# Kernel tuning notes

Measured on AMD Instinct MI355X. Metric: run time of the kernel, lower is better.

Reference implementation:

```python
import jax, jax.numpy as jnp
import numpy as np

SCALE = 2  # init_kwargs scale


def _splits(a, s):
    # (..., W, H) -> (..., W//s, H//s, s*s), matching torch view/permute order
    *lead, W, H = a.shape
    Ws, Hs = W // s, H // s
    n = len(lead)
    b = a.reshape(*lead, s, Ws, s, Hs)
    b = jnp.transpose(b, tuple(range(n)) + (n + 1, n + 3, n, n + 2))
    return b.reshape(*lead, Ws, Hs, s * s)


def _p2o(psf, shape):
    # point-spread-function -> optical transfer function (zero-pad, center-roll, fft2)
    k1, k2 = psf.shape[-2], psf.shape[-1]
    otf = jnp.zeros(psf.shape[:-2] + shape, psf.dtype).at[..., :k1, :k2].set(psf)
    otf = jnp.roll(otf, (-(k1 // 2), -(k2 // 2)), axis=(-2, -1))
    return jnp.fft.fft2(otf, axes=(-2, -1))


def _upsample_zeros(x, s):
    if s == 1:
        return x
    B, C, H, W = x.shape
    return jnp.zeros((B, C, H * s, W * s), x.dtype).at[..., ::s, ::s].set(x)


def setup_inputs() -> dict:
    key = jax.random.key(0)
    k1, k2 = jax.random.split(key)
    B, C, H, W, K = 4, 64, 128, 128, 5
    x = jax.random.normal(k1, (B, C, H, W), jnp.float32)
    w = jax.random.normal(k2, (1, C, K, K), jnp.float32)
    # module init applies softmax over flattened kernel
    weight = jax.nn.softmax(w.reshape(1, C, -1), axis=-1).reshape(1, C, K, K)
    bias = jnp.zeros((1, C, 1, 1), jnp.float32)
    lambda_reg = jnp.full((1, 1, 1, 1), 0.1, jnp.float32)
    return {"x": x, "weight": weight, "bias": bias, "lambda_reg": lambda_reg}


def reference(x, weight, bias, lambda_reg):
    s = SCALE
    _, _, h, w = x.shape
    STy = _upsample_zeros(x, s)                      # [B,C,h*s,w*s] zero-interleaved
    if s != 1:
        x0 = jnp.repeat(jnp.repeat(x, s, axis=-2), s, axis=-1)  # nearest interp
    else:
        x0 = x
    FB = _p2o(weight, (h * s, w * s))                # [1,C,hs,ws] complex
    FBC = jnp.conj(FB)
    F2B = jnp.abs(FB) ** 2
    FBFy = FBC * jnp.fft.fft2(STy, axes=(-2, -1))
    FR = FBFy + jnp.fft.fft2(lambda_reg * x0, axes=(-2, -1))
    FBR = jnp.mean(_splits(FB * FR, s), axis=-1)     # [B,C,h,w] complex
    invW = jnp.mean(_splits(F2B, s), axis=-1)        # [1,C,h,w] real
    lambda_small = lambda_reg                        # scalar lambda: no split needed
    invWBR = FBR / (invW + lambda_small)
    FCBinvWBR = FBC * jnp.tile(invWBR, (1, 1, s, s))
    FX = (FR - FCBinvWBR) / lambda_reg
    out = jnp.real(jnp.fft.ifft2(FX, axes=(-2, -1)))
    return out + bias
```

## Files before the change

kernel.cpp:

```cpp
#include <hip/hip_runtime.h>
#include <math.h>


struct cx { float x, y; };
__device__ __forceinline__ cx cmul(cx a, cx b){ return cx{a.x*b.x - a.y*b.y, a.x*b.y + a.y*b.x}; }
__device__ __forceinline__ cx cadd(cx a, cx b){ return cx{a.x+b.x, a.y+b.y}; }
__device__ __forceinline__ cx csub(cx a, cx b){ return cx{a.x-b.x, a.y-b.y}; }
__device__ __forceinline__ cx cconj(cx a){ return cx{a.x, -a.y}; }
__device__ __forceinline__ cx cscale(cx a, float s){ return cx{a.x*s, a.y*s}; }

__device__ __forceinline__ float2 cmulf(float2 a, float2 b){
    return make_float2(a.x*b.x - a.y*b.y, a.x*b.y + a.y*b.x);
}
__device__ __forceinline__ float2 cmulcf(float2 a, float2 b){
    return make_float2(a.x*b.x + a.y*b.y, a.y*b.x - a.x*b.y);
}
__device__ __forceinline__ float2 caddf(float2 a, float2 b){ return make_float2(a.x+b.x, a.y+b.y); }
__device__ __forceinline__ float2 csubf(float2 a, float2 b){ return make_float2(a.x-b.x, a.y-b.y); }

__device__ __forceinline__ cx conjpair(cx w, float2 A, float2 B){
    return cx{ w.x*(A.x+B.x) + w.y*(A.y-B.y),
               w.x*(A.y+B.y) - w.y*(A.x-B.x) };
}

__device__ __forceinline__ void barrier_lds(){
    __builtin_amdgcn_sched_barrier(0);
    asm volatile("s_waitcnt lgkmcnt(0)" ::: "memory");
    __builtin_amdgcn_s_barrier();
    __builtin_amdgcn_sched_barrier(0);
}

__global__ __launch_bounds__(256)
void precompute_K(const float* __restrict__ weight, const float* __restrict__ lam_ptr,
                  float2* __restrict__ KA, float2* __restrict__ KB)
{
    __shared__ float2 P[5 * 256];

    const int tid  = threadIdx.x;
    const int c    = blockIdx.x >> 5;
    const int slab = blockIdx.x & 31;

    const float* wc = weight + c*25;
    const float lam = lam_ptr[0];
    const float inv_lam = 1.0f / lam;
    const float th  = -6.28318530717958647692f * (1.0f/256.0f);

    {
        float s1,c1, s2,c2;
        __sincosf(th * (float)tid,     &s1, &c1);
        __sincosf(th * (float)(2*tid), &s2, &c2);
        cx er[5] = { cx{c2,-s2}, cx{c1,-s1}, cx{1.f,0.f}, cx{c1,s1}, cx{c2,s2} };
        const int rs = (tid >> 1) | ((tid & 1) << 7);
        #pragma unroll
        for (int a = 0; a < 5; ++a) {
            float px = 0.f, py = 0.f;
            #pragma unroll
            for (int b = 0; b < 5; ++b) {
                float w = wc[a*5 + b];
                px += w * er[b].x;
                py += w * er[b].y;
            }
            P[a*256 + rs] = make_float2(px, py);
        }
    }
    __syncthreads();

    const float scale = 1.0f / 65536.0f;

    #pragma unroll 1
    for (int it = 0; it < 2; ++it) {
        const int p  = slab*512 + it*256 + tid;
        const int qb = p >> 7, rb = p & 127;
        const int q = (int)(__brev((unsigned)qb) >> 25);
        const int r = (int)(__brev((unsigned)rb) >> 25);
        const int rr = (r >> 1) | ((r & 1) << 7);

        float sq1,cq1, sq2,cq2, sr1,cr1;
        __sincosf(th * (float)q,     &sq1, &cq1);
        __sincosf(th * (float)(2*q), &sq2, &cq2);
        __sincosf(th * (float)r,     &sr1, &cr1);
        const cx w1{cq1, sq1};
        const cx w2{cq2, sq2};
        const cx wr{cr1, sr1};

        float2 p0_0 = P[0*256+rr], p1_0 = P[0*256+rr+64];
        float2 p0_1 = P[1*256+rr], p1_1 = P[1*256+rr+64];
        float2 p0_2 = P[2*256+rr], p1_2 = P[2*256+rr+64];
        float2 p0_3 = P[3*256+rr], p1_3 = P[3*256+rr+64];
        float2 p0_4 = P[4*256+rr], p1_4 = P[4*256+rr+64];
        cx B1 = conjpair(w1, p0_1, p0_3);
        cx B2 = conjpair(w2, p0_0, p0_4);
        cx m0 = cx{p0_2.x, p0_2.y};
        cx F00 = cadd(cadd(m0, B1), B2);
        cx F10 = cadd(csub(m0, B1), B2);
        cx D1 = conjpair(w1, p1_1, p1_3);
        cx D2 = conjpair(w2, p1_0, p1_4);
        cx m1 = cx{p1_2.x, p1_2.y};
        cx F01 = cadd(cadd(m1, D1), D2);
        cx F11 = cadd(csub(m1, D1), D2);

        float SF2 = F00.x*F00.x + F00.y*F00.y + F01.x*F01.x + F01.y*F01.y
                  + F10.x*F10.x + F10.y*F10.y + F11.x*F11.x + F11.y*F11.y;
        cx Du0{1.f+cq1,  sq1}, Du1{1.f-cq1, -sq1};
        cx Dv0{1.f+cr1,  sr1}, Dv1{1.f-cr1, -sr1};
        cx T = cadd(cmul(Du0, cadd(cmul(F00,Dv0), cmul(F01,Dv1))),
                    cmul(Du1, cadd(cmul(F10,Dv0), cmul(F11,Dv1))));
        float invW = 0.25f * SF2;
        cx M{invW + 0.25f*lam*T.x, 0.25f*lam*T.y};
        float idn = 1.0f / (invW + lam);
        cx V{M.x*idn, M.y*idn};
        cx W{(1.f - V.x)*inv_lam, -V.y*inv_lam};

        cx Sa = cadd(F00,F01), Sb = cadd(F10,F11);
        cx Da = csub(F00,F01), Db = csub(F10,F11);
        cx C00 = cadd(Sa,Sb), C10 = csub(Sa,Sb);
        cx C01 = cadd(Da,Db), C11 = csub(Da,Db);

        cx WR  = cmul(W,  cconj(wr));
        cx WQ  = cmul(W,  cconj(w1));
        cx WQR = cmul(WQ, cconj(wr));
        cx H0 = cadd(cmul(cconj(C00), W  ), cx{4.f,0.f});
        cx H1 = cadd(cmul(cconj(C01), WR ), cx{4.f,0.f});
        cx H2 = cadd(cmul(cconj(C10), WQ ), cx{4.f,0.f});
        cx H3 = cadd(cmul(cconj(C11), WQR), cx{4.f,0.f});

        float2 kAv = make_float2((H0.x - H1.y)*scale, (H0.y + H1.x)*scale);
        float2 kBv = make_float2((H2.x - H3.y)*scale, (H2.y + H3.x)*scale);
        const int o = (c << 14) + p;
        KA[o] = kAv;
        KB[o] = kBv;
    }
}

#define ST2 129

template<int AXIS> __device__ __forceinline__ int laddr(int line, int i){
    return AXIS ? (i*ST2 + line) : (line*ST2 + i);
}

template<int AXIS, int S>
__device__ __forceinline__ void fwd_pair(float2* Sm, const float2* TW, int tid)
{
    const int h  = 64 >> S;
    const int hh = 32 >> S;
    #pragma unroll
    for (int it = 0; it < 4; ++it) {
        int qid  = it*1024 + tid;
        int line = qid & 127;
        int t    = qid >> 7;
        int blk  = t >> (5 - S);
        int j    = t & (hh - 1);
        int i0   = (blk << (7 - S)) + j;
        int a0 = laddr<AXIS>(line, i0);
        int a1 = laddr<AXIS>(line, i0 + hh);
        int a2 = laddr<AXIS>(line, i0 + h);
        int a3 = laddr<AXIS>(line, i0 + h + hh);
        float2 e0 = Sm[a0], e1 = Sm[a1], e2 = Sm[a2], e3 = Sm[a3];
        float2 w0 = TW[j << S], w1 = TW[(j << S) + 32], w2 = TW[j << (S + 1)];
        float2 u0 = caddf(e0, e2), d0 = cmulf(csubf(e0, e2), w0);
        float2 u1 = caddf(e1, e3), d1 = cmulf(csubf(e1, e3), w1);
        Sm[a0] = caddf(u0, u1);
        Sm[a1] = cmulf(csubf(u0, u1), w2);
        Sm[a2] = caddf(d0, d1);
        Sm[a3] = cmulf(csubf(d0, d1), w2);
    }
}

template<int AXIS, int S>
__device__ __forceinline__ void inv_pair(float2* Sm, const float2* TW, int tid)
{
    const int h = 1 << S;
    #pragma unroll
    for (int it = 0; it < 4; ++it) {
        int qid  = it*1024 + tid;
        int line = qid & 127;
        int t    = qid >> 7;
        int blk  = t >> S;
        int j    = t & (h - 1);
        int base = (blk << (S + 2)) + j;
        int a0 = laddr<AXIS>(line, base);
        int a1 = laddr<AXIS>(line, base + h);
        int a2 = laddr<AXIS>(line, base + 2*h);
        int a3 = laddr<AXIS>(line, base + 3*h);
        float2 e0 = Sm[a0], e1 = Sm[a1], e2 = Sm[a2], e3 = Sm[a3];
        float2 cw0 = TW[j << (6 - S)];
        float2 cw1 = TW[j << (5 - S)];
        float2 cw2 = TW[(j << (5 - S)) + 32];
        float2 t1 = cmulcf(e1, cw0);
        float2 A0 = caddf(e0, t1), A1 = csubf(e0, t1);
        float2 t2 = cmulcf(e3, cw0);
        float2 A2 = caddf(e2, t2), A3 = csubf(e2, t2);
        float2 u = cmulcf(A2, cw1);
        Sm[a0] = caddf(A0, u);
        Sm[a2] = csubf(A0, u);
        float2 v = cmulcf(A3, cw2);
        Sm[a1] = caddf(A1, v);
        Sm[a3] = csubf(A1, v);
    }
}

__global__ __launch_bounds__(1024)
void converse_main(const float* __restrict__ x, const float* __restrict__ bias,
                   const float2* __restrict__ KA, const float2* __restrict__ KB,
                   float* __restrict__ out)
{
    __shared__ float2 S[128 * ST2];
    __shared__ float2 TW[64];
    __shared__ float2 SB[3 * 1024];

    const int tid = threadIdx.x;
    const int bc  = blockIdx.x;
    const int c   = bc & 63;

    if (tid < 64) {
        float s_, c_;
        __sincosf(-6.28318530717958647692f * (float)tid * (1.0f/128.0f), &s_, &c_);
        TW[tid] = make_float2(c_, s_);
    }

    const float* xp = x + (size_t)bc * 16384;
    #pragma unroll
    for (int it = 0; it < 16; ++it) {
        int n = it * 1024 + tid;
        S[(n >> 7) * ST2 + (n & 127)] = make_float2(xp[n], 0.0f);
    }

    const float2* KpA = KA + (size_t)c * 16384;
    const float2* KpB = KB + (size_t)c * 16384;
    const int nn = tid & 127;
    const int t7 = tid >> 7;
    const int kbase = t7*256 + nn;
    float2 kr[16];
    #pragma unroll
    for (int it = 0; it < 8; ++it) {
        kr[2*it]   = KpA[it*2048 + kbase];
        kr[2*it+1] = KpA[it*2048 + kbase + 128];
    }
    barrier_lds();

    fwd_pair<0,0>(S, TW, tid); barrier_lds();
    fwd_pair<0,2>(S, TW, tid); barrier_lds();
    fwd_pair<0,4>(S, TW, tid); barrier_lds();
    #pragma unroll
    for (int it = 0; it < 8; ++it) {
        int g = it*1024 + tid;
        int line = g & 127, k = g >> 7;
        int a = line*ST2 + 2*k;
        float2 u = S[a], v = S[a+1];
        S[a]   = caddf(u, v);
        S[a+1] = csubf(u, v);
    }
    barrier_lds();

    fwd_pair<1,0>(S, TW, tid); barrier_lds();
    fwd_pair<1,2>(S, TW, tid); barrier_lds();
    fwd_pair<1,4>(S, TW, tid); barrier_lds();

    const float bv = bias[c];
    float* op = out + (size_t)bc * 65536;

    float2 sA[8], sB[5];
    #pragma unroll
    for (int it = 0; it < 8; ++it) {
        int j = it*8 + t7;
        int a = (2*j)*ST2 + nn;
        float2 u = S[a], v = S[a + ST2];
        float2 vA = caddf(u, v);
        float2 vB = csubf(u, v);
        sA[it] = vA;
        if (it < 5) sB[it] = vB;
        else        SB[(it-5)*1024 + tid] = vB;
        float2 w0 = cmulf(vA, kr[2*it]);
        float2 w1 = cmulf(vB, kr[2*it+1]);
        S[a]       = caddf(w0, w1);
        S[a + ST2] = csubf(w0, w1);
    }
    barrier_lds();

    inv_pair<1,1>(S, TW, tid); barrier_lds();
    inv_pair<1,3>(S, TW, tid); barrier_lds();
    inv_pair<1,5>(S, TW, tid); barrier_lds();
    inv_pair<0,0>(S, TW, tid); barrier_lds();
    inv_pair<0,2>(S, TW, tid); barrier_lds();
    inv_pair<0,4>(S, TW, tid); barrier_lds();

    #pragma unroll
    for (int it = 0; it < 8; ++it) {
        int g = it*1024 + tid;
        int j = g & 63, m = g >> 6;
        int a = m*ST2 + j;
        float2 u = S[a], v = S[a + 64];
        float2 t = cmulcf(v, TW[j]);
        float2 o0 = caddf(u, t);
        float2 o1 = csubf(u, t);
        size_t ro = (size_t)(2*m) * 256;
        *(float2*)(op + ro + 2*j)       = make_float2(o0.x + bv, o0.y + bv);
        *(float2*)(op + ro + 2*j + 128) = make_float2(o1.x + bv, o1.y + bv);
    }
    barrier_lds();

    #pragma unroll
    for (int it = 0; it < 8; ++it) {
        int j = it*8 + t7;
        float2 kb0 = KpB[it*2048 + kbase];
        float2 kb1 = KpB[it*2048 + kbase + 128];
        float2 vB = (it < 5) ? sB[it] : SB[(it-5)*1024 + tid];
        float2 w0 = cmulf(sA[it], kb0);
        float2 w1 = cmulf(vB, kb1);
        int a = (2*j)*ST2 + nn;
        S[a]       = caddf(w0, w1);
        S[a + ST2] = csubf(w0, w1);
    }
    barrier_lds();

    inv_pair<1,1>(S, TW, tid); barrier_lds();
    inv_pair<1,3>(S, TW, tid); barrier_lds();
    inv_pair<1,5>(S, TW, tid); barrier_lds();
    inv_pair<0,0>(S, TW, tid); barrier_lds();
    inv_pair<0,2>(S, TW, tid); barrier_lds();
    inv_pair<0,4>(S, TW, tid); barrier_lds();

    #pragma unroll
    for (int it = 0; it < 8; ++it) {
        int g = it*1024 + tid;
        int j = g & 63, m = g >> 6;
        int a = m*ST2 + j;
        float2 u = S[a], v = S[a + 64];
        float2 t = cmulcf(v, TW[j]);
        float2 o0 = caddf(u, t);
        float2 o1 = csubf(u, t);
        size_t ro = (size_t)(2*m + 1) * 256;
        *(float2*)(op + ro + 2*j)       = make_float2(o0.x + bv, o0.y + bv);
        *(float2*)(op + ro + 2*j + 128) = make_float2(o1.x + bv, o1.y + bv);
    }
}

extern "C" void kernel_launch(void* const* d_in, const int* in_sizes, int n_in,
                              void* d_out, int out_size, void* d_ws, size_t ws_size,
                              hipStream_t stream)
{
    const float* x      = (const float*)d_in[0];
    const float* weight = (const float*)d_in[1];
    const float* bias   = (const float*)d_in[2];
    const float* lam    = (const float*)d_in[3];
    float* out = (float*)d_out;

    float2* KA = (float2*)d_ws;
    float2* KB = KA + (size_t)64 * 16384;

    hipLaunchKernelGGL(precompute_K, dim3(2048), dim3(256), 0, stream,
                       weight, lam, KA, KB);
    hipLaunchKernelGGL(converse_main, dim3(256), dim3(1024), 0, stream,
                       x, bias, KA, KB, out);
}
```

Measured before the change: 131.3 us.

## Fuse spectral kernel precompute into main FFT kernel, recomputing per block

Removes the separate precompute_K launch and its global KA/KB workspace. Each block of the main kernel now builds the per-channel weight partial sums and a 256-entry twiddle table in shared memory, then computes kernel values inline during each pointwise multiply. This drops the second launch and the 16 MB workspace write and read. In exchange each of the 256 blocks redoes the filter arithmetic, which was previously shared across the 4 batches of a channel, so the main kernel does more ALU work. The spill split of sB also moves from 5 register slots to 6.

After: 161.8 us. +23.2%, slower.

```diff
diff --git a/kernel.cpp b/kernel.cpp
--- a/kernel.cpp
+++ b/kernel.cpp
@@ -7,7 +7,6 @@
 __device__ __forceinline__ cx cadd(cx a, cx b){ return cx{a.x+b.x, a.y+b.y}; }
 __device__ __forceinline__ cx csub(cx a, cx b){ return cx{a.x-b.x, a.y-b.y}; }
 __device__ __forceinline__ cx cconj(cx a){ return cx{a.x, -a.y}; }
-__device__ __forceinline__ cx cscale(cx a, float s){ return cx{a.x*s, a.y*s}; }
 
 __device__ __forceinline__ float2 cmulf(float2 a, float2 b){
     return make_float2(a.x*b.x - a.y*b.y, a.x*b.y + a.y*b.x);
@@ -30,105 +29,60 @@
     __builtin_amdgcn_sched_barrier(0);
 }
 
-__global__ __launch_bounds__(256)
-void precompute_K(const float* __restrict__ weight, const float* __restrict__ lam_ptr,
-                  float2* __restrict__ KA, float2* __restrict__ KB)
-{
-    __shared__ float2 P[5 * 256];
-
-    const int tid  = threadIdx.x;
-    const int c    = blockIdx.x >> 5;
-    const int slab = blockIdx.x & 31;
-
-    const float* wc = weight + c*25;
-    const float lam = lam_ptr[0];
-    const float inv_lam = 1.0f / lam;
-    const float th  = -6.28318530717958647692f * (1.0f/256.0f);
-
-    {
-        float s1,c1, s2,c2;
-        __sincosf(th * (float)tid,     &s1, &c1);
-        __sincosf(th * (float)(2*tid), &s2, &c2);
-        cx er[5] = { cx{c2,-s2}, cx{c1,-s1}, cx{1.f,0.f}, cx{c1,s1}, cx{c2,s2} };
-        const int rs = (tid >> 1) | ((tid & 1) << 7);
-        #pragma unroll
-        for (int a = 0; a < 5; ++a) {
-            float px = 0.f, py = 0.f;
-            #pragma unroll
-            for (int b = 0; b < 5; ++b) {
-                float w = wc[a*5 + b];
-                px += w * er[b].x;
-                py += w * er[b].y;
-            }
-            P[a*256 + rs] = make_float2(px, py);
-        }
-    }
-    __syncthreads();
-
-    const float scale = 1.0f / 65536.0f;
-
-    #pragma unroll 1
-    for (int it = 0; it < 2; ++it) {
-        const int p  = slab*512 + it*256 + tid;
-        const int qb = p >> 7, rb = p & 127;
-        const int q = (int)(__brev((unsigned)qb) >> 25);
-        const int r = (int)(__brev((unsigned)rb) >> 25);
-        const int rr = (r >> 1) | ((r & 1) << 7);
-
-        float sq1,cq1, sq2,cq2, sr1,cr1;
-        __sincosf(th * (float)q,     &sq1, &cq1);
-        __sincosf(th * (float)(2*q), &sq2, &cq2);
-        __sincosf(th * (float)r,     &sr1, &cr1);
-        const cx w1{cq1, sq1};
-        const cx w2{cq2, sq2};
-        const cx wr{cr1, sr1};
-
-        float2 p0_0 = P[0*256+rr], p1_0 = P[0*256+rr+64];
-        float2 p0_1 = P[1*256+rr], p1_1 = P[1*256+rr+64];
-        float2 p0_2 = P[2*256+rr], p1_2 = P[2*256+rr+64];
-        float2 p0_3 = P[3*256+rr], p1_3 = P[3*256+rr+64];
-        float2 p0_4 = P[4*256+rr], p1_4 = P[4*256+rr+64];
-        cx B1 = conjpair(w1, p0_1, p0_3);
-        cx B2 = conjpair(w2, p0_0, p0_4);
-        cx m0 = cx{p0_2.x, p0_2.y};
-        cx F00 = cadd(cadd(m0, B1), B2);
-        cx F10 = cadd(csub(m0, B1), B2);
-        cx D1 = conjpair(w1, p1_1, p1_3);
-        cx D2 = conjpair(w2, p1_0, p1_4);
-        cx m1 = cx{p1_2.x, p1_2.y};
-        cx F01 = cadd(cadd(m1, D1), D2);
-        cx F11 = cadd(csub(m1, D1), D2);
-
-        float SF2 = F00.x*F00.x + F00.y*F00.y + F01.x*F01.x + F01.y*F01.y
-                  + F10.x*F10.x + F10.y*F10.y + F11.x*F11.x + F11.y*F11.y;
-        cx Du0{1.f+cq1,  sq1}, Du1{1.f-cq1, -sq1};
-        cx Dv0{1.f+cr1,  sr1}, Dv1{1.f-cr1, -sr1};
-        cx T = cadd(cmul(Du0, cadd(cmul(F00,Dv0), cmul(F01,Dv1))),
-                    cmul(Du1, cadd(cmul(F10,Dv0), cmul(F11,Dv1))));
-        float invW = 0.25f * SF2;
-        cx M{invW + 0.25f*lam*T.x, 0.25f*lam*T.y};
-        float idn = 1.0f / (invW + lam);
-        cx V{M.x*idn, M.y*idn};
-        cx W{(1.f - V.x)*inv_lam, -V.y*inv_lam};
-
-        cx Sa = cadd(F00,F01), Sb = cadd(F10,F11);
-        cx Da = csub(F00,F01), Db = csub(F10,F11);
-        cx C00 = cadd(Sa,Sb), C10 = csub(Sa,Sb);
-        cx C01 = cadd(Da,Db), C11 = csub(Da,Db);
-
-        cx WR  = cmul(W,  cconj(wr));
+template<int PASS>
+__device__ __forceinline__ float2 kval(int q, const float2* __restrict__ TAB,
+                                       const float2* __restrict__ P, int rr,
+                                       cx wr, cx Dv0, cx Dv1,
+                                       float lam, float inv_lam, float scale)
+{
+    float2 w1f = TAB[q];
+    float2 w2f = TAB[(2*q) & 255];
+    cx w1{w1f.x, w1f.y}, w2{w2f.x, w2f.y};
+
+    float2 p00 = P[0*256+rr], p10 = P[0*256+rr+64];
+    float2 p01 = P[1*256+rr], p11 = P[1*256+rr+64];
+    float2 p02 = P[2*256+rr], p12 = P[2*256+rr+64];
+    float2 p03 = P[3*256+rr], p13 = P[3*256+rr+64];
+    float2 p04 = P[4*256+rr], p14 = P[4*256+rr+64];
+
+    cx B1 = conjpair(w1, p01, p03);
+    cx B2 = conjpair(w2, p00, p04);
+    cx m0 = cx{p02.x, p02.y};
+    cx F00 = cadd(cadd(m0, B1), B2);
+    cx F10 = cadd(csub(m0, B1), B2);
+    cx D1 = conjpair(w1, p11, p13);
+    cx D2 = conjpair(w2, p10, p14);
+    cx m1 = cx{p12.x, p12.y};
+    cx F01 = cadd(cadd(m1, D1), D2);
+    cx F11 = cadd(csub(m1, D1), D2);
+
+    float SF2 = F00.x*F00.x + F00.y*F00.y + F01.x*F01.x + F01.y*F01.y
+              + F10.x*F10.x + F10.y*F10.y + F11.x*F11.x + F11.y*F11.y;
+    cx Du0{1.f+w1.x,  w1.y}, Du1{1.f-w1.x, -w1.y};
+    cx T = cadd(cmul(Du0, cadd(cmul(F00,Dv0), cmul(F01,Dv1))),
+                cmul(Du1, cadd(cmul(F10,Dv0), cmul(F11,Dv1))));
+    float invW = 0.25f * SF2;
+    cx M{invW + 0.25f*lam*T.x, 0.25f*lam*T.y};
+    float idn = 1.0f / (invW + lam);
+    cx V{M.x*idn, M.y*idn};
+    cx W{(1.f - V.x)*inv_lam, -V.y*inv_lam};
+
+    cx Sa = cadd(F00,F01), Sb = cadd(F10,F11);
+    cx Da = csub(F00,F01), Db = csub(F10,F11);
+
+    if (PASS == 0) {
+        cx C00 = cadd(Sa,Sb), C01 = cadd(Da,Db);
+        cx WR  = cmul(W, cconj(wr));
+        cx H0 = cadd(cmul(cconj(C00), W ), cx{4.f,0.f});
+        cx H1 = cadd(cmul(cconj(C01), WR), cx{4.f,0.f});
+        return make_float2((H0.x - H1.y)*scale, (H0.y + H1.x)*scale);
+    } else {
+        cx C10 = csub(Sa,Sb), C11 = csub(Da,Db);
         cx WQ  = cmul(W,  cconj(w1));
         cx WQR = cmul(WQ, cconj(wr));
-        cx H0 = cadd(cmul(cconj(C00), W  ), cx{4.f,0.f});
-        cx H1 = cadd(cmul(cconj(C01), WR ), cx{4.f,0.f});
         cx H2 = cadd(cmul(cconj(C10), WQ ), cx{4.f,0.f});
         cx H3 = cadd(cmul(cconj(C11), WQR), cx{4.f,0.f});
-
-        float2 kAv = make_float2((H0.x - H1.y)*scale, (H0.y + H1.x)*scale);
-        float2 kBv = make_float2((H2.x - H3.y)*scale, (H2.y + H3.x)*scale);
-        const int o = (c << 14) + p;
-        KA[o] = kAv;
-        KB[o] = kBv;
+        return make_float2((H2.x - H3.y)*scale, (H2.y + H3.x)*scale);
     }
 }
 
@@ -200,41 +154,56 @@
 }
 
 __global__ __launch_bounds__(1024)
-void converse_main(const float* __restrict__ x, const float* __restrict__ bias,
-                   const float2* __restrict__ KA, const float2* __restrict__ KB,
-                   float* __restrict__ out)
+void converse_fused(const float* __restrict__ x, const float* __restrict__ weight,
+                    const float* __restrict__ bias, const float* __restrict__ lam_ptr,
+                    float* __restrict__ out)
 {
     __shared__ float2 S[128 * ST2];
     __shared__ float2 TW[64];
-    __shared__ float2 SB[3 * 1024];
+    __shared__ float2 TAB[256];
+    __shared__ float2 P[5 * 256];
+    __shared__ float2 SB[2 * 1024];
 
     const int tid = threadIdx.x;
     const int bc  = blockIdx.x;
     const int c   = bc & 63;
+
+    const float lam = lam_ptr[0];
+    const float inv_lam = 1.0f / lam;
+    const float th = -6.28318530717958647692f * (1.0f/256.0f);
+    const float scale = 1.0f / 65536.0f;
 
     if (tid < 64) {
         float s_, c_;
         __sincosf(-6.28318530717958647692f * (float)tid * (1.0f/128.0f), &s_, &c_);
         TW[tid] = make_float2(c_, s_);
     }
+    if (tid < 256) {
+        float s1, c1_, s2, c2_;
+        __sincosf(th * (float)tid,     &s1, &c1_);
+        __sincosf(th * (float)(2*tid), &s2, &c2_);
+        TAB[tid] = make_float2(c1_, s1);
+        cx er[5] = { cx{c2_,-s2}, cx{c1_,-s1}, cx{1.f,0.f}, cx{c1_,s1}, cx{c2_,s2} };
+        const float* wc = weight + c*25;
+        const int rs = (tid >> 1) | ((tid & 1) << 7);
+        #pragma unroll
+        for (int a = 0; a < 5; ++a) {
+            float px = 0.f, py = 0.f;
+            #pragma unroll
+            for (int b = 0; b < 5; ++b) {
+                float w = wc[a*5 + b];
+                px += w * er[b].x;
+                py += w * er[b].y;
+            }
+            P[a*256 + rs] = make_float2(px, py);
+        }
+    }
 
     const float* xp = x + (size_t)bc * 16384;
     #pragma unroll
     for (int it = 0; it < 16; ++it) {
         int n = it * 1024 + tid;
         S[(n >> 7) * ST2 + (n & 127)] = make_float2(xp[n], 0.0f);
-    }
-
-    const float2* KpA = KA + (size_t)c * 16384;
-    const float2* KpB = KB + (size_t)c * 16384;
-    const int nn = tid & 127;
-    const int t7 = tid >> 7;
-    const int kbase = t7*256 + nn;
-    float2 kr[16];
-    #pragma unroll
-    for (int it = 0; it < 8; ++it) {
-        kr[2*it]   = KpA[it*2048 + kbase];
-        kr[2*it+1] = KpA[it*2048 + kbase + 128];
     }
     barrier_lds();
 
@@ -259,19 +228,31 @@
     const float bv = bias[c];
     float* op = out + (size_t)bc * 65536;
 
-    float2 sA[8], sB[5];
+    const int nn = tid & 127;
+    const int t7 = tid >> 7;
+    const int r  = (int)(__brev((unsigned)nn) >> 25);
+    const int rr = (r >> 1) | ((r & 1) << 7);
+    const float2 wrf = TAB[r];
+    const cx wr{wrf.x, wrf.y};
+    const cx Dv0{1.f+wr.x,  wr.y}, Dv1{1.f-wr.x, -wr.y};
+
+    float2 sA[8], sB[6];
     #pragma unroll
     for (int it = 0; it < 8; ++it) {
         int j = it*8 + t7;
+        int q1 = (int)(__brev((unsigned)(2*j))   >> 25);
+        int q2 = (int)(__brev((unsigned)(2*j+1)) >> 25);
+        float2 kA0 = kval<0>(q1, TAB, P, rr, wr, Dv0, Dv1, lam, inv_lam, scale);
+        float2 kA1 = kval<0>(q2, TAB, P, rr, wr, Dv0, Dv1, lam, inv_lam, scale);
         int a = (2*j)*ST2 + nn;
         float2 u = S[a], v = S[a + ST2];
         float2 vA = caddf(u, v);
         float2 vB = csubf(u, v);
         sA[it] = vA;
-        if (it < 5) sB[it] = vB;
-        else        SB[(it-5)*1024 + tid] = vB;
-        float2 w0 = cmulf(vA, kr[2*it]);
-        float2 w1 = cmulf(vB, kr[2*it+1]);
+        if (it < 6) sB[it] = vB;
+        else        SB[(it-6)*1024 + tid] = vB;
+        float2 w0 = cmulf(vA, kA0);
+        float2 w1 = cmulf(vB, kA1);
         S[a]       = caddf(w0, w1);
         S[a + ST2] = csubf(w0, w1);
     }
@@ -302,11 +283,13 @@
     #pragma unroll
     for (int it = 0; it < 8; ++it) {
         int j = it*8 + t7;
-        float2 kb0 = KpB[it*2048 + kbase];
-        float2 kb1 = KpB[it*2048 + kbase + 128];
-        float2 vB = (it < 5) ? sB[it] : SB[(it-5)*1024 + tid];
-        float2 w0 = cmulf(sA[it], kb0);
-        float2 w1 = cmulf(vB, kb1);
+        int q1 = (int)(__brev((unsigned)(2*j))   >> 25);
+        int q2 = (int)(__brev((unsigned)(2*j+1)) >> 25);
+        float2 kB0 = kval<1>(q1, TAB, P, rr, wr, Dv0, Dv1, lam, inv_lam, scale);
+        float2 kB1 = kval<1>(q2, TAB, P, rr, wr, Dv0, Dv1, lam, inv_lam, scale);
+        float2 vB = (it < 6) ? sB[it] : SB[(it-6)*1024 + tid];
+        float2 w0 = cmulf(sA[it], kB0);
+        float2 w1 = cmulf(vB, kB1);
         int a = (2*j)*ST2 + nn;
         S[a]       = caddf(w0, w1);
         S[a + ST2] = csubf(w0, w1);
@@ -345,11 +328,6 @@
     const float* lam    = (const float*)d_in[3];
     float* out = (float*)d_out;
 
-    float2* KA = (float2*)d_ws;
-    float2* KB = KA + (size_t)64 * 16384;
-
-    hipLaunchKernelGGL(precompute_K, dim3(2048), dim3(256), 0, stream,
-                       weight, lam, KA, KB);
-    hipLaunchKernelGGL(converse_main, dim3(256), dim3(1024), 0, stream,
-                       x, bias, KA, KB, out);
-}
+    hipLaunchKernelGGL(converse_fused, dim3(256), dim3(1024), 0, stream,
+                       x, weight, bias, lam, out);
+}
```

## Switch LDS FFT passes from radix-4 to radix-8/16 to cut barriers

Applied to the files above, without the earlier changes.

Replaces the radix-4 pair passes in the shared-memory 2D FFT with radix-8 and radix-16 passes, so each thread does more butterflies in registers per pass. This cuts the forward FFT from seven passes and barriers to four, and each inverse FFT from six to four, which reduces LDS round trips and synchronisation. It also moves the KA kernel loads from an up-front register array into the multiply loop, which lowers register pressure but exposes global load latency at that point. The larger per-thread register arrays may raise VGPR usage at 1024 threads per block.

Measured after the change: 128.7 us. 1.02x faster.

```diff
diff --git a/kernel.cpp b/kernel.cpp
--- a/kernel.cpp
+++ b/kernel.cpp
@@ -7,7 +7,6 @@
 __device__ __forceinline__ cx cadd(cx a, cx b){ return cx{a.x+b.x, a.y+b.y}; }
 __device__ __forceinline__ cx csub(cx a, cx b){ return cx{a.x-b.x, a.y-b.y}; }
 __device__ __forceinline__ cx cconj(cx a){ return cx{a.x, -a.y}; }
-__device__ __forceinline__ cx cscale(cx a, float s){ return cx{a.x*s, a.y*s}; }
 
 __device__ __forceinline__ float2 cmulf(float2 a, float2 b){
     return make_float2(a.x*b.x - a.y*b.y, a.x*b.y + a.y*b.x);
@@ -139,63 +138,131 @@
 }
 
 template<int AXIS, int S>
-__device__ __forceinline__ void fwd_pair(float2* Sm, const float2* TW, int tid)
-{
-    const int h  = 64 >> S;
-    const int hh = 32 >> S;
-    #pragma unroll
-    for (int it = 0; it < 4; ++it) {
+__device__ __forceinline__ void fwd_oct(float2* Sm, const float2* TW, int tid)
+{
+    const int hhh = 16 >> S;
+    #pragma unroll
+    for (int it = 0; it < 2; ++it) {
         int qid  = it*1024 + tid;
         int line = qid & 127;
         int t    = qid >> 7;
-        int blk  = t >> (5 - S);
-        int j    = t & (hh - 1);
+        int j    = t & (hhh - 1);
+        int blk  = t >> (4 - S);
         int i0   = (blk << (7 - S)) + j;
-        int a0 = laddr<AXIS>(line, i0);
-        int a1 = laddr<AXIS>(line, i0 + hh);
-        int a2 = laddr<AXIS>(line, i0 + h);
-        int a3 = laddr<AXIS>(line, i0 + h + hh);
-        float2 e0 = Sm[a0], e1 = Sm[a1], e2 = Sm[a2], e3 = Sm[a3];
-        float2 w0 = TW[j << S], w1 = TW[(j << S) + 32], w2 = TW[j << (S + 1)];
-        float2 u0 = caddf(e0, e2), d0 = cmulf(csubf(e0, e2), w0);
-        float2 u1 = caddf(e1, e3), d1 = cmulf(csubf(e1, e3), w1);
-        Sm[a0] = caddf(u0, u1);
-        Sm[a1] = cmulf(csubf(u0, u1), w2);
-        Sm[a2] = caddf(d0, d1);
-        Sm[a3] = cmulf(csubf(d0, d1), w2);
-    }
+        float2 f[8];
+        #pragma unroll
+        for (int k = 0; k < 8; ++k) f[k] = Sm[laddr<AXIS>(line, i0 + k*hhh)];
+        #pragma unroll
+        for (int k = 0; k < 4; ++k) {
+            float2 a = f[k], b = f[k+4];
+            f[k]   = caddf(a, b);
+            f[k+4] = cmulf(csubf(a, b), TW[(j << S) + k*16]);
+        }
+        #pragma unroll
+        for (int h8 = 0; h8 < 8; h8 += 4)
+          #pragma unroll
+          for (int k = 0; k < 2; ++k) {
+            float2 a = f[h8+k], b = f[h8+k+2];
+            f[h8+k]   = caddf(a, b);
+            f[h8+k+2] = cmulf(csubf(a, b), TW[(j << (S+1)) + k*32]);
+          }
+        float2 wC = TW[j << (S+2)];
+        #pragma unroll
+        for (int h4 = 0; h4 < 8; h4 += 2) {
+            float2 a = f[h4], b = f[h4+1];
+            f[h4]   = caddf(a, b);
+            f[h4+1] = cmulf(csubf(a, b), wC);
+        }
+        #pragma unroll
+        for (int k = 0; k < 8; ++k) Sm[laddr<AXIS>(line, i0 + k*hhh)] = f[k];
+    }
+}
+
+template<int AXIS>
+__device__ __forceinline__ void fwd_oct16(float2* Sm, const float2* TW, int tid)
+{
+    int line = tid & 127;
+    int g    = tid >> 7;
+    int i0   = g * 16;
+    float2 f[16];
+    #pragma unroll
+    for (int k = 0; k < 16; ++k) f[k] = Sm[laddr<AXIS>(line, i0 + k)];
+    #pragma unroll
+    for (int k = 0; k < 8; ++k) {
+        float2 a = f[k], b = f[k+8];
+        f[k]   = caddf(a, b);
+        f[k+8] = cmulf(csubf(a, b), TW[k << 3]);
+    }
+    #pragma unroll
+    for (int h = 0; h < 16; h += 8)
+      #pragma unroll
+      for (int k = 0; k < 4; ++k) {
+        float2 a = f[h+k], b = f[h+k+4];
+        f[h+k]   = caddf(a, b);
+        f[h+k+4] = cmulf(csubf(a, b), TW[k << 4]);
+      }
+    #pragma unroll
+    for (int h = 0; h < 16; h += 4)
+      #pragma unroll
+      for (int k = 0; k < 2; ++k) {
+        float2 a = f[h+k], b = f[h+k+2];
+        f[h+k]   = caddf(a, b);
+        f[h+k+2] = cmulf(csubf(a, b), TW[k << 5]);
+      }
+    #pragma unroll
+    for (int h = 0; h < 16; h += 2) {
+        float2 a = f[h], b = f[h+1];
+        f[h]   = caddf(a, b);
+        f[h+1] = csubf(a, b);
+    }
+    #pragma unroll
+    for (int k = 0; k < 16; ++k) Sm[laddr<AXIS>(line, i0 + k)] = f[k];
 }
 
 template<int AXIS, int S>
-__device__ __forceinline__ void inv_pair(float2* Sm, const float2* TW, int tid)
+__device__ __forceinline__ void inv_oct(float2* Sm, const float2* TW, int tid)
 {
     const int h = 1 << S;
     #pragma unroll
-    for (int it = 0; it < 4; ++it) {
+    for (int it = 0; it < 2; ++it) {
         int qid  = it*1024 + tid;
         int line = qid & 127;
         int t    = qid >> 7;
+        int j    = t & (h - 1);
         int blk  = t >> S;
-        int j    = t & (h - 1);
-        int base = (blk << (S + 2)) + j;
-        int a0 = laddr<AXIS>(line, base);
-        int a1 = laddr<AXIS>(line, base + h);
-        int a2 = laddr<AXIS>(line, base + 2*h);
-        int a3 = laddr<AXIS>(line, base + 3*h);
-        float2 e0 = Sm[a0], e1 = Sm[a1], e2 = Sm[a2], e3 = Sm[a3];
-        float2 cw0 = TW[j << (6 - S)];
-        float2 cw1 = TW[j << (5 - S)];
-        float2 cw2 = TW[(j << (5 - S)) + 32];
-        float2 t1 = cmulcf(e1, cw0);
-        float2 A0 = caddf(e0, t1), A1 = csubf(e0, t1);
-        float2 t2 = cmulcf(e3, cw0);
-        float2 A2 = caddf(e2, t2), A3 = csubf(e2, t2);
-        float2 u = cmulcf(A2, cw1);
-        Sm[a0] = caddf(A0, u);
-        Sm[a2] = csubf(A0, u);
-        float2 v = cmulcf(A3, cw2);
-        Sm[a1] = caddf(A1, v);
-        Sm[a3] = csubf(A1, v);
+        int base = (blk << (S + 3)) + j;
+        float2 f[8];
+        #pragma unroll
+        for (int k = 0; k < 8; ++k) f[k] = Sm[laddr<AXIS>(line, base + k*h)];
+        float2 cwA = TW[j << (6 - S)];
+        #pragma unroll
+        for (int i = 0; i < 4; ++i) {
+            float2 a = f[2*i], b = cmulcf(f[2*i+1], cwA);
+            f[2*i]   = caddf(a, b);
+            f[2*i+1] = csubf(a, b);
+        }
+        float2 cwB0 = TW[j << (5 - S)];
+        float2 cwB1 = TW[(j << (5 - S)) + 32];
+        #pragma unroll
+        for (int hb = 0; hb < 8; hb += 4) {
+            float2 u = cmulcf(f[hb+2], cwB0);
+            float2 a0 = f[hb+0];
+            f[hb+0] = caddf(a0, u);
+            f[hb+2] = csubf(a0, u);
+            float2 v = cmulcf(f[hb+3], cwB1);
+            float2 a1 = f[hb+1];
+            f[hb+1] = caddf(a1, v);
+            f[hb+3] = csubf(a1, v);
+        }
+        #pragma unroll
+        for (int k = 0; k < 4; ++k) {
+            float2 w = cmulcf(f[k+4], TW[(j << (4 - S)) + k*16]);
+            float2 a = f[k];
+            f[k]   = caddf(a, w);
+            f[k+4] = csubf(a, w);
+        }
+        #pragma unroll
+        for (int k = 0; k < 8; ++k) Sm[laddr<AXIS>(line, base + k*h)] = f[k];
     }
 }
 
@@ -224,45 +291,28 @@
         int n = it * 1024 + tid;
         S[(n >> 7) * ST2 + (n & 127)] = make_float2(xp[n], 0.0f);
     }
-
+    barrier_lds();
+
+    fwd_oct<0,0>(S, TW, tid);  barrier_lds();
+    fwd_oct16<0>(S, TW, tid);  barrier_lds();
+
+    fwd_oct<1,0>(S, TW, tid);  barrier_lds();
+    fwd_oct<1,3>(S, TW, tid);  barrier_lds();
+
+    const float bv = bias[c];
+    float* op = out + (size_t)bc * 65536;
     const float2* KpA = KA + (size_t)c * 16384;
     const float2* KpB = KB + (size_t)c * 16384;
     const int nn = tid & 127;
     const int t7 = tid >> 7;
     const int kbase = t7*256 + nn;
-    float2 kr[16];
-    #pragma unroll
-    for (int it = 0; it < 8; ++it) {
-        kr[2*it]   = KpA[it*2048 + kbase];
-        kr[2*it+1] = KpA[it*2048 + kbase + 128];
-    }
-    barrier_lds();
-
-    fwd_pair<0,0>(S, TW, tid); barrier_lds();
-    fwd_pair<0,2>(S, TW, tid); barrier_lds();
-    fwd_pair<0,4>(S, TW, tid); barrier_lds();
-    #pragma unroll
-    for (int it = 0; it < 8; ++it) {
-        int g = it*1024 + tid;
-        int line = g & 127, k = g >> 7;
-        int a = line*ST2 + 2*k;
-        float2 u = S[a], v = S[a+1];
-        S[a]   = caddf(u, v);
-        S[a+1] = csubf(u, v);
-    }
-    barrier_lds();
-
-    fwd_pair<1,0>(S, TW, tid); barrier_lds();
-    fwd_pair<1,2>(S, TW, tid); barrier_lds();
-    fwd_pair<1,4>(S, TW, tid); barrier_lds();
-
-    const float bv = bias[c];
-    float* op = out + (size_t)bc * 65536;
 
     float2 sA[8], sB[5];
     #pragma unroll
     for (int it = 0; it < 8; ++it) {
         int j = it*8 + t7;
+        float2 kA0 = KpA[it*2048 + kbase];
+        float2 kA1 = KpA[it*2048 + kbase + 128];
         int a = (2*j)*ST2 + nn;
         float2 u = S[a], v = S[a + ST2];
         float2 vA = caddf(u, v);
@@ -270,19 +320,17 @@
         sA[it] = vA;
         if (it < 5) sB[it] = vB;
         else        SB[(it-5)*1024 + tid] = vB;
-        float2 w0 = cmulf(vA, kr[2*it]);
-        float2 w1 = cmulf(vB, kr[2*it+1]);
+        float2 w0 = cmulf(vA, kA0);
+        float2 w1 = cmulf(vB, kA1);
         S[a]       = caddf(w0, w1);
         S[a + ST2] = csubf(w0, w1);
     }
     barrier_lds();
 
-    inv_pair<1,1>(S, TW, tid); barrier_lds();
-    inv_pair<1,3>(S, TW, tid); barrier_lds();
-    inv_pair<1,5>(S, TW, tid); barrier_lds();
-    inv_pair<0,0>(S, TW, tid); barrier_lds();
-    inv_pair<0,2>(S, TW, tid); barrier_lds();
-    inv_pair<0,4>(S, TW, tid); barrier_lds();
+    inv_oct<1,1>(S, TW, tid); barrier_lds();
+    inv_oct<1,4>(S, TW, tid); barrier_lds();
+    inv_oct<0,0>(S, TW, tid); barrier_lds();
+    inv_oct<0,3>(S, TW, tid); barrier_lds();
 
     #pragma unroll
     for (int it = 0; it < 8; ++it) {
@@ -302,23 +350,21 @@
     #pragma unroll
     for (int it = 0; it < 8; ++it) {
         int j = it*8 + t7;
-        float2 kb0 = KpB[it*2048 + kbase];
-        float2 kb1 = KpB[it*2048 + kbase + 128];
+        float2 kB0 = KpB[it*2048 + kbase];
+        float2 kB1 = KpB[it*2048 + kbase + 128];
         float2 vB = (it < 5) ? sB[it] : SB[(it-5)*1024 + tid];
-        float2 w0 = cmulf(sA[it], kb0);
-        float2 w1 = cmulf(vB, kb1);
+        float2 w0 = cmulf(sA[it], kB0);
+        float2 w1 = cmulf(vB, kB1);
         int a = (2*j)*ST2 + nn;
         S[a]       = caddf(w0, w1);
         S[a + ST2] = csubf(w0, w1);
     }
     barrier_lds();
 
-    inv_pair<1,1>(S, TW, tid); barrier_lds();
-    inv_pair<1,3>(S, TW, tid); barrier_lds();
-    inv_pair<1,5>(S, TW, tid); barrier_lds();
-    inv_pair<0,0>(S, TW, tid); barrier_lds();
-    inv_pair<0,2>(S, TW, tid); barrier_lds();
-    inv_pair<0,4>(S, TW, tid); barrier_lds();
+    inv_oct<1,1>(S, TW, tid); barrier_lds();
+    inv_oct<1,4>(S, TW, tid); barrier_lds();
+    inv_oct<0,0>(S, TW, tid); barrier_lds();
+    inv_oct<0,3>(S, TW, tid); barrier_lds();
 
     #pragma unroll
     for (int it = 0; it < 8; ++it) {
```
